# Performance work log

Measured on AMD Instinct MI355X. Metric: run time of the kernel, lower is better.

Reference implementation:

```python
import jax, jax.numpy as jnp
import numpy as np

C_NUM, D_NUM = 64, 128
N_NODES = C_NUM * D_NUM + C_NUM + D_NUM  # 8384
HEADS, OUT = 4, 256


def gat_conv(h, src, dst, W, al, ar, b):
    """DGL-style GATConv (eval mode, attn_drop off). h:[N,F], W:[F,H*O], al/ar:[H,O], b:[H*O]."""
    N = h.shape[0]
    H, O = al.shape
    feat = (h @ W).reshape(N, H, O)
    el = jnp.sum(feat * al, axis=-1)                      # [N,H]
    er = jnp.sum(feat * ar, axis=-1)
    e = jax.nn.leaky_relu(el[src] + er[dst], 0.2)         # [E,H]
    m = jax.ops.segment_max(e, dst, num_segments=N)
    m = jnp.where(jnp.isfinite(m), m, 0.0)
    p = jnp.exp(e - m[dst])
    s = jax.ops.segment_sum(p, dst, num_segments=N)
    a = p / jnp.maximum(s[dst], 1e-9)                     # edge softmax per dst, per head
    out = jax.ops.segment_sum(a[:, :, None] * feat[src], dst, num_segments=N)  # [N,H,O]
    return out + b.reshape(1, H, O)


def cagat_layer(edges, dfeat, cvec, gw, al, ar, gb,
                wq_w, wq_b, wk_w, wk_b, wv_w, wv_b, ip_w, ip_b, op_w, op_b):
    ch = cvec.shape[1]
    pad = jnp.repeat(cvec, D_NUM, axis=0)                       # [c*d, ch]
    pad3 = jnp.broadcast_to(cvec.mean(axis=0), (D_NUM, ch))      # [d, ch]
    cfin = jnp.concatenate([pad, cvec, pad3], axis=0)            # [N, ch]
    inf = jnp.concatenate([dfeat, cfin], axis=1)                 # [N, F+ch]
    # 4 relation-specific GATConvs, stacked (HeteroGraphConv aggregate='stack')
    rst = jnp.stack([gat_conv(inf, edges[t, 0], edges[t, 1], gw[t], al[t], ar[t], gb[t])
                     for t in range(4)], axis=1)                 # [N,4,H,O]
    N = inf.shape[0]
    rst = rst.reshape(N, 4 * HEADS, OUT)
    E = OUT
    Q = (cfin @ wq_w + wq_b)[:, None, :]                         # [N,1,E]
    K = rst @ wk_w + wk_b                                        # [N,16,E]
    V = rst @ wv_w + wv_b
    # nn.MultiheadAttention(E, 1): in-proj then single-head SDPA then out-proj
    q = Q @ ip_w[:E].T + ip_b[:E]
    k = K @ ip_w[E:2 * E].T + ip_b[E:2 * E]
    v = V @ ip_w[2 * E:].T + ip_b[2 * E:]
    att = jax.nn.softmax(jnp.einsum('nqe,nke->nqk', q, k) / jnp.sqrt(jnp.float32(E)), axis=-1)
    o = jnp.einsum('nqk,nke->nqe', att, v) @ op_w.T + op_b
    return o.reshape(N, E)


def setup_inputs() -> dict:
    key = jax.random.key(0)
    ks = iter(jax.random.split(key, 64))
    rn = lambda shape: jax.random.normal(next(ks), shape, jnp.float32) * 0.05
    inp = {}
    inp['x'] = rn((D_NUM, 256))
    inp['cf'] = rn((C_NUM, 512))
    inp['cf_net_w'] = rn((512, 128)); inp['cf_net_b'] = rn((128,))
    inp['ht_w'] = rn((512, 256)); inp['ht_b'] = rn((256,))
    for l in ('1', '2'):
        inp['gw' + l] = rn((4, 384, HEADS * OUT))
        inp['al' + l] = rn((4, HEADS, OUT))
        inp['ar' + l] = rn((4, HEADS, OUT))
        inp['gb' + l] = rn((4, HEADS * OUT))
        inp['wq' + l + '_w'] = rn((128, 256)); inp['wq' + l + '_b'] = rn((256,))
        inp['wk' + l + '_w'] = rn((256, 256)); inp['wk' + l + '_b'] = rn((256,))
        inp['wv' + l + '_w'] = rn((256, 256)); inp['wv' + l + '_b'] = rn((256,))
        inp['ip' + l + '_w'] = rn((768, 256)); inp['ip' + l + '_b'] = rn((768,))
        inp['op' + l + '_w'] = rn((256, 256)); inp['op' + l + '_b'] = rn((256,))
    inp['edges'] = jax.random.randint(next(ks), (4, 2, 50000), 0, N_NODES, dtype=jnp.int32)
    return inp


def reference(x, cf, cf_net_w, cf_net_b, ht_w, ht_b,
              gw1, al1, ar1, gb1, wq1_w, wq1_b, wk1_w, wk1_b, wv1_w, wv1_b, ip1_w, ip1_b, op1_w, op1_b,
              gw2, al2, ar2, gb2, wq2_w, wq2_b, wk2_w, wk2_b, wv2_w, wv2_b, ip2_w, ip2_b, op2_w, op2_b,
              edges):
    cf_vec = cf @ cf_net_w + cf_net_b                           # [c, cell_hidden]
    d_pad = jnp.tile(x, (C_NUM, 1))                             # [c*d, in]
    d_uc = cf @ ht_w + ht_b                                     # [c, in]
    d_feat = jnp.concatenate([d_pad, d_uc, x], axis=0)          # [N, in]
    h = cagat_layer(edges, d_feat, cf_vec, gw1, al1, ar1, gb1,
                    wq1_w, wq1_b, wk1_w, wk1_b, wv1_w, wv1_b, ip1_w, ip1_b, op1_w, op1_b)
    h = cagat_layer(edges, h, cf_vec, gw2, al2, ar2, gb2,
                    wq2_w, wq2_b, wk2_w, wk2_b, wv2_w, wv2_b, ip2_w, ip2_b, op2_w, op2_b)
    return h
```

## Files before the change

### kernel.cpp

```cpp
#include <hip/hip_runtime.h>
#include <hip/hip_bf16.h>

typedef __hip_bfloat16 bf16;
typedef __attribute__((ext_vector_type(8))) short short8;
typedef __attribute__((ext_vector_type(4))) short short4v;
typedef __attribute__((ext_vector_type(4))) float f32x4;

#define KN 8384
#define KNPAD 8448
#define KE 50000
#define NBIG 4480

__device__ __forceinline__ float toF(float v){ return v; }
__device__ __forceinline__ float toF(bf16 v){ return __bfloat162float(v); }
__device__ __forceinline__ float b2f(short u){ return __uint_as_float(((unsigned int)(unsigned short)u) << 16); }
__device__ __forceinline__ void stor(float* p, float v){ *p = v; }
__device__ __forceinline__ void stor(bf16* p, float v){ *p = __float2bfloat16(v); }

__device__ __forceinline__ void glds16(const bf16* g, bf16* l){
  __builtin_amdgcn_global_load_lds(
      (const __attribute__((address_space(1))) unsigned int*)(g),
      (__attribute__((address_space(3))) unsigned int*)(l), 16, 0, 0);
}

template<typename TC>
__global__ __launch_bounds__(256)
void gemm_mfma_bt(const bf16* __restrict__ A, const bf16* __restrict__ BT,
                  const float* __restrict__ bias, TC* __restrict__ C,
                  int M, int N, int K, int ldc, int nbx)
{
  __shared__ bf16 As[3][128 * 32];
  __shared__ bf16 Bs[3][128 * 32];
  const int nwg = gridDim.x;
  const int q = nwg >> 3, r = nwg & 7;
  const int xcd = blockIdx.x & 7, idx = blockIdx.x >> 3;
  const int sw = (xcd < r) ? xcd * (q + 1) + idx : r * (q + 1) + (xcd - r) * q + idx;
  const int bn = (sw % nbx) * 128, bm = (sw / nbx) * 128;
  const int tid = threadIdx.x;
  const int w = tid >> 6, l = tid & 63;
  const int wr = (w >> 1) * 64, wc = (w & 1) * 64;
  const int lr = l & 15;
  int rS[2], lqS[2];
  #pragma unroll
  for (int i = 0; i < 2; i++){
    rS[i] = w * 32 + i * 16 + (l >> 2);
    lqS[i] = (l & 3) ^ ((rS[i] >> 1) & 3);
  }
  const bf16* gA0 = A  + (size_t)(bm + rS[0]) * K + lqS[0] * 8;
  const bf16* gA1 = A  + (size_t)(bm + rS[1]) * K + lqS[1] * 8;
  const bf16* gB0 = BT + (size_t)(bn + rS[0]) * K + lqS[0] * 8;
  const bf16* gB1 = BT + (size_t)(bn + rS[1]) * K + lqS[1] * 8;
  const int nt = K >> 5;
  auto issue = [&](int t){
    int b = t - (t / 3) * 3;
    int k0 = t << 5;
    glds16(gA0 + k0, &As[b][w * 1024]);
    glds16(gA1 + k0, &As[b][w * 1024 + 512]);
    glds16(gB0 + k0, &Bs[b][w * 1024]);
    glds16(gB1 + k0, &Bs[b][w * 1024 + 512]);
  };
  f32x4 acc[4][4] = {};
  issue(0);
  issue(1);
  for (int t = 0; t < nt; t++){
    if (t < nt - 1) asm volatile("s_waitcnt vmcnt(4)\ns_barrier" ::: "memory");
    else            asm volatile("s_waitcnt vmcnt(0)\ns_barrier" ::: "memory");
    int b = t - (t / 3) * 3;
    short8 a[4], bb[4];
    #pragma unroll
    for (int i = 0; i < 4; i++){
      int R = wr + i * 16 + lr;
      int pq = (l >> 4) ^ ((R >> 1) & 3);
      a[i] = *(short8*)&As[b][R * 32 + pq * 8];
    }
    #pragma unroll
    for (int j = 0; j < 4; j++){
      int R = wc + j * 16 + lr;
      int pq = (l >> 4) ^ ((R >> 1) & 3);
      bb[j] = *(short8*)&Bs[b][R * 32 + pq * 8];
    }
    #pragma unroll
    for (int i = 0; i < 4; i++)
      #pragma unroll
      for (int j = 0; j < 4; j++)
        acc[i][j] = __builtin_amdgcn_mfma_f32_16x16x32_bf16(a[i], bb[j], acc[i][j], 0, 0, 0);
    if (t + 2 < nt) issue(t + 2);
  }
  const int orow = (l >> 4) * 4, ocol = l & 15;
  #pragma unroll
  for (int i = 0; i < 4; i++){
    #pragma unroll
    for (int j = 0; j < 4; j++){
      int gcol = bn + wc + j * 16 + ocol;
      float bv = bias ? bias[gcol] : 0.f;
      #pragma unroll
      for (int rg = 0; rg < 4; rg++){
        int grow = bm + wr + i * 16 + orow + rg;
        if (grow < M) stor(&C[(size_t)grow * ldc + gcol], acc[i][j][rg] + bv);
      }
    }
  }
}

__global__ void k_transGW(const float* __restrict__ gw, bf16* __restrict__ bigBT){
  __shared__ float t[32][33];
  int rel = blockIdx.z;
  const float* B = gw + (size_t)rel * 384 * 1024;
  bf16* BT = bigBT + (size_t)rel * 1024 * 384;
  int n0 = blockIdx.x * 32, k0 = blockIdx.y * 32;
  int tx = threadIdx.x, ty = threadIdx.y;
  for (int i = ty; i < 32; i += 8)
    t[i][tx] = B[(size_t)(k0 + i) * 1024 + n0 + tx];
  __syncthreads();
  for (int i = ty; i < 32; i += 8)
    BT[(size_t)(n0 + i) * 384 + k0 + tx] = __float2bfloat16(t[tx][i]);
}

__global__ __launch_bounds__(256)
void k_galr(const float* __restrict__ gw, const float* __restrict__ al,
            const float* __restrict__ ar, bf16* __restrict__ bigBT){
  int r = blockIdx.y;
  int k = blockIdx.x * 4 + (threadIdx.x >> 6);
  int lane = threadIdx.x & 63;
  int rr = r & 15, t = rr >> 2, h = rr & 3;
  const float* wsrc = ((r < 16) ? al : ar) + t * 1024 + h * 256;
  const float* gp = gw + (size_t)t * 384 * 1024 + (size_t)k * 1024 + h * 256;
  float v = 0.f;
  #pragma unroll
  for (int i = 0; i < 4; i++){
    int o = lane + i * 64;
    v += gp[o] * wsrc[o];
  }
  #pragma unroll
  for (int off = 32; off; off >>= 1) v += __shfl_down(v, off);
  if (lane == 0) bigBT[(size_t)(4352 + r) * 384 + k] = __float2bfloat16(v);
}

__global__ void k_zpad(bf16* bigBT){
  int i = blockIdx.x * blockDim.x + threadIdx.x;
  if (i < 96 * 384) bigBT[(size_t)4384 * 384 + i] = __float2bfloat16(0.f);
}

__global__ void k_wprep(const float* __restrict__ ipw, const float* __restrict__ wkw,
                        const float* __restrict__ opw, const float* __restrict__ wvw,
                        float* __restrict__ ipwQT, float* __restrict__ wkwT,
                        float* __restrict__ opwT, float* __restrict__ wvwT){
  __shared__ float t[32][33];
  const float* S; float* D;
  switch (blockIdx.z){
    case 0: S = ipw; D = ipwQT; break;
    case 1: S = wkw; D = wkwT; break;
    case 2: S = opw; D = opwT; break;
    default: S = wvw; D = wvwT; break;
  }
  int c0 = blockIdx.x * 32, r0 = blockIdx.y * 32;
  int tx = threadIdx.x, ty = threadIdx.y;
  for (int i = ty; i < 32; i += 8)
    t[i][tx] = S[(size_t)(r0 + i) * 256 + c0 + tx];
  __syncthreads();
  for (int i = ty; i < 32; i += 8)
    D[(size_t)(c0 + i) * 256 + r0 + tx] = t[tx][i];
}

__global__ __launch_bounds__(256)
void k_fold1(const float* __restrict__ wqw, const float* __restrict__ wqb,
             const float* __restrict__ ipw, const float* __restrict__ ipb,
             const float* __restrict__ ipwQT, const float* __restrict__ wkwT,
             const float* __restrict__ opwT,
             float* __restrict__ Wq, float* __restrict__ B2,
             float* __restrict__ M1, float* __restrict__ bq){
  int b = blockIdx.x, tid = threadIdx.x;
  if (b < 128){
    int c = b; float s = 0.f;
    for (int e = 0; e < 256; e++) s += wqw[c * 256 + e] * ipwQT[e * 256 + tid];
    Wq[c * 256 + tid] = s;
  } else if (b < 384){
    int j = b - 128; float s = 0.f;
    for (int e = 0; e < 256; e++) s += wkwT[e * 256 + tid] * ipw[(256 + j) * 256 + e];
    B2[j * 256 + tid] = s;
  } else if (b < 640){
    int e = b - 384; float s = 0.f;
    for (int f = 0; f < 256; f++) s += ipw[(512 + f) * 256 + e] * opwT[f * 256 + tid];
    M1[e * 256 + tid] = s;
  } else {
    float s = 0.f;
    for (int e = 0; e < 256; e++) s += wqb[e] * ipwQT[e * 256 + tid];
    bq[tid] = s + ipb[tid];
  }
}

__global__ __launch_bounds__(256)
void k_fold2(const float* __restrict__ Wq, const float* __restrict__ B2,
             const float* __restrict__ M1, const float* __restrict__ bq,
             const float* __restrict__ wvb, const float* __restrict__ ipb,
             const float* __restrict__ opb,
             const float* __restrict__ wvwT, const float* __restrict__ opwT,
             bf16* __restrict__ bigBT, bf16* __restrict__ WvT,
             float* __restrict__ bv, float* __restrict__ biasc){
  int b = blockIdx.x, tid = threadIdx.x;
  if (b < 256){
    int d = b; float s = 0.f;
    for (int j = 0; j < 256; j++) s += Wq[d * 256 + j] * B2[j * 256 + tid];
    bigBT[(size_t)(4096 + tid) * 384 + 256 + d] = __float2bfloat16(s);
  } else if (b < 512){
    int j = b - 256; float s = 0.f;
    for (int e = 0; e < 256; e++) s += wvwT[e * 256 + tid] * M1[e * 256 + j];
    WvT[j * 256 + tid] = __float2bfloat16(s);
  } else {
    float b2 = 0.f;
    for (int j = 0; j < 256; j++) b2 += bq[j] * B2[j * 256 + tid];
    float s = 0.f;
    for (int e = 0; e < 256; e++) s += wvb[e] * M1[e * 256 + tid];
    for (int f = 0; f < 256; f++) s += ipb[512 + f] * opwT[f * 256 + tid];
    bv[tid] = s + opb[tid];
    for (int i = tid; i < NBIG; i += 256)
      biasc[i] = (i - 4096 == tid) ? b2 : 0.f;
    for (int k = 0; k < 256; k++)
      bigBT[(size_t)(4096 + tid) * 384 + k] = __float2bfloat16(0.f);
  }
}

__global__ __launch_bounds__(384)
void k_pre(const float* __restrict__ cf, const float* __restrict__ cfw, const float* __restrict__ cfb,
           const float* __restrict__ htw, const float* __restrict__ htb,
           float* __restrict__ cfvec, float* __restrict__ duc)
{
  int c = blockIdx.x;
  int col = threadIdx.x;
  __shared__ float row[512];
  for (int i = col; i < 512; i += 384) row[i] = cf[c * 512 + i];
  __syncthreads();
  if (col < 128){
    float acc = cfb[col];
    for (int k = 0; k < 512; k++) acc += row[k] * cfw[k * 128 + col];
    cfvec[c * 128 + col] = acc;
  } else {
    int j = col - 128;
    float acc = htb[j];
    for (int k = 0; k < 512; k++) acc += row[k] * htw[k * 256 + j];
    duc[c * 256 + j] = acc;
  }
}
__global__ void k_mean(const float* cv, float* m){
  int o = threadIdx.x;
  float s = 0.f;
  for (int c = 0; c < 64; c++) s += cv[c * 128 + o];
  m[o] = s * (1.f / 64.f);
}
__global__ __launch_bounds__(384)
void k_infasm(const float* __restrict__ x, const float* __restrict__ duc,
              const float* __restrict__ cv, const float* __restrict__ cm,
              bf16* __restrict__ inf){
  int n = blockIdx.x, o = threadIdx.x;
  float v;
  if (o < 256){
    if (n < 8192)      v = x[(n & 127) * 256 + o];
    else if (n < 8256) v = duc[(n - 8192) * 256 + o];
    else               v = x[(n - 8256) * 256 + o];
  } else {
    int oo = o - 256;
    if (n < 8192)      v = cv[(n >> 7) * 128 + oo];
    else if (n < 8256) v = cv[(n - 8192) * 128 + oo];
    else               v = cm[oo];
  }
  inf[(size_t)n * 384 + o] = __float2bfloat16(v);
}
__global__ void k_zeroi(int* p, int n){
  int i = blockIdx.x * blockDim.x + threadIdx.x; if (i < n) p[i] = 0;
}
__global__ void k_copyi(const int* a, int* b, int n){
  int i = blockIdx.x * blockDim.x + threadIdx.x; if (i < n) b[i] = a[i];
}
__global__ void k_countB(const int* __restrict__ edges, int* __restrict__ cnt){
  int i = blockIdx.x * blockDim.x + threadIdx.x;
  if (i < 4 * KE){
    int t = i / KE, idx = i - t * KE;
    int d = edges[t * 2 * KE + KE + idx];
    atomicAdd(&cnt[t * KN + d], 1);
  }
}
__global__ void k_fillB(const int* __restrict__ edges, int* __restrict__ cur, int* __restrict__ csrc){
  int i = blockIdx.x * blockDim.x + threadIdx.x;
  if (i < 4 * KE){
    int t = i / KE, idx = i - t * KE;
    int s = edges[t * 2 * KE + idx];
    int d = edges[t * 2 * KE + KE + idx];
    int p = atomicAdd(&cur[t * KN + d], 1);
    csrc[p] = s;
  }
}
__global__ void k_scan(const int* __restrict__ cnt, int* __restrict__ ptr, int n){
  __shared__ int part[1024];
  int tid = threadIdx.x;
  const int CH = (n + 1023) >> 10;
  int base = tid * CH;
  int s = 0;
  for (int i = 0; i < CH; i++){ int idx = base + i; if (idx < n) s += cnt[idx]; }
  part[tid] = s; __syncthreads();
  for (int off = 1; off < 1024; off <<= 1){
    int v = (tid >= off) ? part[tid - off] : 0;
    __syncthreads();
    part[tid] += v;
    __syncthreads();
  }
  int run = part[tid] - s;
  for (int i = 0; i < CH; i++){
    int idx = base + i;
    if (idx < n){ ptr[idx] = run; run += cnt[idx]; }
  }
  if (tid == 1023) ptr[n] = part[1023];
}

__global__ __launch_bounds__(256)
void k_aggattn(const int* __restrict__ ptr, const int* __restrict__ csrc,
               const bf16* __restrict__ big, const float* __restrict__ gb,
               bf16* __restrict__ rbar)
{
  const int n = blockIdx.x, tid = threadIdx.x;
  const int w = tid >> 6, lane = tid & 63;
  const int t = w;
  const int head = lane >> 4;
  __shared__ float s_rst[16][260];
  __shared__ float s_sc[16];
  __shared__ float sa4[4][64][4];
  __shared__ int ssrcW[4][64];
  const int beg = ptr[t * KN + n], deg = ptr[t * KN + n + 1] - beg;
  short4v e4 = *(const short4v*)&big[(size_t)n * NBIG + 4368 + t * 4];
  float ern[4] = {b2f(e4[0]), b2f(e4[1]), b2f(e4[2]), b2f(e4[3])};
  float sums[4] = {0.f, 0.f, 0.f, 0.f};
  for (int j = lane; j < deg; j += 64){
    int s = csrc[beg + j];
    short4v l4 = *(const short4v*)&big[(size_t)s * NBIG + 4352 + t * 4];
    #pragma unroll
    for (int h = 0; h < 4; h++){
      float e = b2f(l4[h]) + ern[h];
      e = e > 0.f ? e : 0.2f * e;
      sums[h] += __expf(e);
    }
  }
  #pragma unroll
  for (int off = 32; off; off >>= 1){
    #pragma unroll
    for (int h = 0; h < 4; h++) sums[h] += __shfl_xor(sums[h], off);
  }
  float sinv[4];
  #pragma unroll
  for (int h = 0; h < 4; h++) sinv[h] = 1.f / fmaxf(sums[h], 1e-9f);
  float acc[16];
  #pragma unroll
  for (int i = 0; i < 16; i++) acc[i] = 0.f;
  const size_t cbase = (size_t)t * 1024 + lane * 16;
  for (int c0 = 0; c0 < deg; c0 += 64){
    int cn = min(64, deg - c0);
    if (lane < cn){
      int s = csrc[beg + c0 + lane];
      ssrcW[t][lane] = s;
      short4v l4 = *(const short4v*)&big[(size_t)s * NBIG + 4352 + t * 4];
      #pragma unroll
      for (int h = 0; h < 4; h++){
        float e = b2f(l4[h]) + ern[h];
        e = e > 0.f ? e : 0.2f * e;
        sa4[t][lane][h] = __expf(e) * sinv[h];
      }
    }
    for (int j = 0; j < cn; j++){
      int s = ssrcW[t][j];
      float wj = sa4[t][j][head];
      const bf16* fp = &big[(size_t)s * NBIG + cbase];
      short8 v0 = *(const short8*)fp;
      short8 v1 = *(const short8*)(fp + 8);
      #pragma unroll
      for (int i = 0; i < 8; i++) acc[i] += wj * b2f(v0[i]);
      #pragma unroll
      for (int i = 0; i < 8; i++) acc[8 + i] += wj * b2f(v1[i]);
    }
  }
  {
    const float* gbp = gb + t * 1024 + lane * 16;
    float* rp = &s_rst[t * 4 + head][(lane & 15) * 16];
    #pragma unroll
    for (int i = 0; i < 16; i++) rp[i] = acc[i] + gbp[i];
  }
  __syncthreads();
  const bf16* q = big + (size_t)n * NBIG + 4096;
  #pragma unroll
  for (int si = 0; si < 4; si++){
    int s = w * 4 + si;
    float v = 0.f;
    #pragma unroll
    for (int i = 0; i < 4; i++){
      int o = lane + i * 64;
      v += s_rst[s][o] * toF(q[o]);
    }
    #pragma unroll
    for (int off = 32; off; off >>= 1) v += __shfl_down(v, off);
    if (lane == 0) s_sc[s] = v * 0.0625f;
  }
  __syncthreads();
  float sc[16]; float m = -1e30f;
  #pragma unroll
  for (int s = 0; s < 16; s++){ sc[s] = s_sc[s]; m = fmaxf(m, sc[s]); }
  float sum = 0.f;
  #pragma unroll
  for (int s = 0; s < 16; s++){ sc[s] = __expf(sc[s] - m); sum += sc[s]; }
  float inv = 1.f / sum;
  float r = 0.f;
  #pragma unroll
  for (int s = 0; s < 16; s++) r += sc[s] * s_rst[s][tid];
  rbar[(size_t)n * 256 + tid] = __float2bfloat16(r * inv);
}

struct LWT {
  const float *gw, *al, *ar, *gb, *wqw, *wqb, *wkw, *wkb, *wvw, *wvb, *ipw, *ipb, *opw, *opb;
};

extern "C" void kernel_launch(void* const* d_in, const int* in_sizes, int n_in,
                              void* d_out, int out_size, void* d_ws, size_t ws_size,
                              hipStream_t stream)
{
  const float* x   = (const float*)d_in[0];
  const float* cf  = (const float*)d_in[1];
  const float* cfw = (const float*)d_in[2];
  const float* cfb = (const float*)d_in[3];
  const float* htw = (const float*)d_in[4];
  const float* htb = (const float*)d_in[5];
  LWT L[2];
  for (int l = 0; l < 2; l++){
    int b = 6 + l * 14;
    L[l].gw  = (const float*)d_in[b + 0];
    L[l].al  = (const float*)d_in[b + 1];
    L[l].ar  = (const float*)d_in[b + 2];
    L[l].gb  = (const float*)d_in[b + 3];
    L[l].wqw = (const float*)d_in[b + 4];
    L[l].wqb = (const float*)d_in[b + 5];
    L[l].wkw = (const float*)d_in[b + 6];
    L[l].wkb = (const float*)d_in[b + 7];
    L[l].wvw = (const float*)d_in[b + 8];
    L[l].wvb = (const float*)d_in[b + 9];
    L[l].ipw = (const float*)d_in[b + 10];
    L[l].ipb = (const float*)d_in[b + 11];
    L[l].opw = (const float*)d_in[b + 12];
    L[l].opb = (const float*)d_in[b + 13];
  }
  const int* edges = (const int*)d_in[34];

  char* w = (char*)d_ws;
  size_t off = 0;
  auto alc = [&](size_t bytes) -> void* {
    off = (off + 255) & ~(size_t)255;
    void* p = w + off; off += bytes; return p;
  };
  float* f_cfvec = (float*)alc(64 * 128 * 4);
  float* f_cfmean= (float*)alc(128 * 4);
  float* f_duc   = (float*)alc(64 * 256 * 4);
  bf16*  b_inf   = (bf16*) alc((size_t)KNPAD * 384 * 2);
  bf16*  b_big   = (bf16*) alc((size_t)KN * NBIG * 2);
  bf16*  b_bigBT = (bf16*) alc((size_t)NBIG * 384 * 2);
  float* f_biasc = (float*)alc((size_t)NBIG * 4);
  bf16*  b_rbar  = (bf16*) alc((size_t)KNPAD * 256 * 2);
  float* f_Wq    = (float*)alc(128 * 256 * 4);
  float* f_B2    = (float*)alc(256 * 256 * 4);
  float* f_M1    = (float*)alc(256 * 256 * 4);
  float* f_bq    = (float*)alc(256 * 4);
  float* f_bv    = (float*)alc(256 * 4);
  bf16*  b_WvT   = (bf16*) alc(256 * 256 * 2);
  float* f_ipwQT = (float*)alc(256 * 256 * 4);
  float* f_wkwT  = (float*)alc(256 * 256 * 4);
  float* f_opwT  = (float*)alc(256 * 256 * 4);
  float* f_wvwT  = (float*)alc(256 * 256 * 4);
  int*   i_ptr   = (int*)  alc((size_t)(4 * KN + 1) * 4);
  int*   i_src   = (int*)  alc((size_t)4 * KE * 4);
  int*   i_cnt   = (int*)  alc((size_t)4 * KN * 4);
  int*   i_cur   = (int*)  alc((size_t)4 * KN * 4);
  if (off > ws_size) return;

  k_pre<<<64, 384, 0, stream>>>(cf, cfw, cfb, htw, htb, f_cfvec, f_duc);
  k_mean<<<1, 128, 0, stream>>>(f_cfvec, f_cfmean);
  k_infasm<<<KN, 384, 0, stream>>>(x, f_duc, f_cfvec, f_cfmean, b_inf);
  k_zpad<<<(96 * 384 + 255) / 256, 256, 0, stream>>>(b_bigBT);

  k_zeroi<<<(4 * KN + 255) / 256, 256, 0, stream>>>(i_cnt, 4 * KN);
  k_countB<<<(4 * KE + 255) / 256, 256, 0, stream>>>(edges, i_cnt);
  k_scan<<<1, 1024, 0, stream>>>(i_cnt, i_ptr, 4 * KN);
  k_copyi<<<(4 * KN + 255) / 256, 256, 0, stream>>>(i_ptr, i_cur, 4 * KN);
  k_fillB<<<(4 * KE + 255) / 256, 256, 0, stream>>>(edges, i_cur, i_src);

  auto run_layer = [&](const LWT& Wt, bool last){
    k_transGW<<<dim3(32, 12, 4), dim3(32, 8), 0, stream>>>(Wt.gw, b_bigBT);
    k_galr<<<dim3(96, 32), 256, 0, stream>>>(Wt.gw, Wt.al, Wt.ar, b_bigBT);
    k_wprep<<<dim3(8, 8, 4), dim3(32, 8), 0, stream>>>(Wt.ipw, Wt.wkw, Wt.opw, Wt.wvw,
                                                       f_ipwQT, f_wkwT, f_opwT, f_wvwT);
    k_fold1<<<641, 256, 0, stream>>>(Wt.wqw, Wt.wqb, Wt.ipw, Wt.ipb,
                                     f_ipwQT, f_wkwT, f_opwT,
                                     f_Wq, f_B2, f_M1, f_bq);
    k_fold2<<<513, 256, 0, stream>>>(f_Wq, f_B2, f_M1, f_bq, Wt.wvb, Wt.ipb, Wt.opb,
                                     f_wvwT, f_opwT,
                                     b_bigBT, b_WvT, f_bv, f_biasc);
    gemm_mfma_bt<bf16><<<(NBIG / 128) * 66, 256, 0, stream>>>(
        b_inf, b_bigBT, f_biasc, b_big, KN, NBIG, 384, NBIG, NBIG / 128);
    k_aggattn<<<KN, 256, 0, stream>>>(i_ptr, i_src, b_big, Wt.gb, b_rbar);
    if (last)
      gemm_mfma_bt<float><<<2 * 66, 256, 0, stream>>>(
          b_rbar, b_WvT, f_bv, (float*)d_out, KN, 256, 256, 256, 2);
    else
      gemm_mfma_bt<bf16><<<2 * 66, 256, 0, stream>>>(
          b_rbar, b_WvT, f_bv, b_inf, KN, 256, 256, 384, 2);
  };

  run_layer(L[0], false);
  run_layer(L[1], true);
}
```

Baseline: 545.4 us.

## Batch both layers' weight prep into merged kernels and unroll edge aggregation

The transpose, al/ar projection, zero-padding and weight-transpose kernels are merged into one `k_prep_all` launch. That launch, plus the fold kernels, now covers both layers at once through a z-dimension over separate per-layer buffers, so all weight preprocessing runs up front with fewer launches. The GEMM K-loop issues the next async LDS load right after the barrier, before the MFMAs, to overlap more. The CSR cursor copy is folded into the scan kernel. The edge gather in aggregation is unrolled by 4 to keep more loads in flight, and `k_fold2` caches a `Wq` row in shared memory. The cost is extra workspace for duplicated per-layer weight buffers.

```diff
diff --git a/kernel.cpp b/kernel.cpp
--- a/kernel.cpp
+++ b/kernel.cpp
@@ -65,6 +65,7 @@
   for (int t = 0; t < nt; t++){
     if (t < nt - 1) asm volatile("s_waitcnt vmcnt(4)\ns_barrier" ::: "memory");
     else            asm volatile("s_waitcnt vmcnt(0)\ns_barrier" ::: "memory");
+    if (t + 2 < nt) issue(t + 2);
     int b = t - (t / 3) * 3;
     short8 a[4], bb[4];
     #pragma unroll
@@ -84,7 +85,6 @@
       #pragma unroll
       for (int j = 0; j < 4; j++)
         acc[i][j] = __builtin_amdgcn_mfma_f32_16x16x32_bf16(a[i], bb[j], acc[i][j], 0, 0, 0);
-    if (t + 2 < nt) issue(t + 2);
   }
   const int orow = (l >> 4) * 4, ocol = l & 15;
   #pragma unroll
@@ -102,121 +102,129 @@
   }
 }
 
-__global__ void k_transGW(const float* __restrict__ gw, bf16* __restrict__ bigBT){
-  __shared__ float t[32][33];
-  int rel = blockIdx.z;
-  const float* B = gw + (size_t)rel * 384 * 1024;
-  bf16* BT = bigBT + (size_t)rel * 1024 * 384;
-  int n0 = blockIdx.x * 32, k0 = blockIdx.y * 32;
-  int tx = threadIdx.x, ty = threadIdx.y;
-  for (int i = ty; i < 32; i += 8)
-    t[i][tx] = B[(size_t)(k0 + i) * 1024 + n0 + tx];
-  __syncthreads();
-  for (int i = ty; i < 32; i += 8)
-    BT[(size_t)(n0 + i) * 384 + k0 + tx] = __float2bfloat16(t[tx][i]);
-}
-
+struct LPtrs {
+  const float *gw[2], *al[2], *ar[2];
+  const float *wqw[2], *wqb[2], *wkw[2], *wvw[2], *wvb[2];
+  const float *ipw[2], *ipb[2], *opw[2], *opb[2];
+  bf16* bigBT[2];
+  float *ipwQT[2], *wkwT[2], *opwT[2], *wvwT[2];
+  float *Wq[2], *B2[2], *M1[2], *bq[2];
+  bf16* WvT[2];
+  float *bv[2], *biasc[2];
+};
+
+#define PT0 1536
+#define PT1 4608
+#define PT2 4864
+#define PT3 5248
+#define PT4 5392
 __global__ __launch_bounds__(256)
-void k_galr(const float* __restrict__ gw, const float* __restrict__ al,
-            const float* __restrict__ ar, bf16* __restrict__ bigBT){
-  int r = blockIdx.y;
-  int k = blockIdx.x * 4 + (threadIdx.x >> 6);
-  int lane = threadIdx.x & 63;
-  int rr = r & 15, t = rr >> 2, h = rr & 3;
-  const float* wsrc = ((r < 16) ? al : ar) + t * 1024 + h * 256;
-  const float* gp = gw + (size_t)t * 384 * 1024 + (size_t)k * 1024 + h * 256;
-  float v = 0.f;
-  #pragma unroll
-  for (int i = 0; i < 4; i++){
-    int o = lane + i * 64;
-    v += gp[o] * wsrc[o];
-  }
-  #pragma unroll
-  for (int off = 32; off; off >>= 1) v += __shfl_down(v, off);
-  if (lane == 0) bigBT[(size_t)(4352 + r) * 384 + k] = __float2bfloat16(v);
-}
-
-__global__ void k_zpad(bf16* bigBT){
-  int i = blockIdx.x * blockDim.x + threadIdx.x;
-  if (i < 96 * 384) bigBT[(size_t)4384 * 384 + i] = __float2bfloat16(0.f);
-}
-
-__global__ void k_wprep(const float* __restrict__ ipw, const float* __restrict__ wkw,
-                        const float* __restrict__ opw, const float* __restrict__ wvw,
-                        float* __restrict__ ipwQT, float* __restrict__ wkwT,
-                        float* __restrict__ opwT, float* __restrict__ wvwT){
-  __shared__ float t[32][33];
-  const float* S; float* D;
-  switch (blockIdx.z){
-    case 0: S = ipw; D = ipwQT; break;
-    case 1: S = wkw; D = wkwT; break;
-    case 2: S = opw; D = opwT; break;
-    default: S = wvw; D = wvwT; break;
-  }
-  int c0 = blockIdx.x * 32, r0 = blockIdx.y * 32;
-  int tx = threadIdx.x, ty = threadIdx.y;
-  for (int i = ty; i < 32; i += 8)
-    t[i][tx] = S[(size_t)(r0 + i) * 256 + c0 + tx];
-  __syncthreads();
-  for (int i = ty; i < 32; i += 8)
-    D[(size_t)(c0 + i) * 256 + r0 + tx] = t[tx][i];
+void k_prep_all(LPtrs P){
+  const int lay = blockIdx.z;
+  const int b = blockIdx.x, tid = threadIdx.x;
+  bf16* bigBT = P.bigBT[lay];
+  if (b < PT0){
+    __shared__ float t[32][33];
+    int rel = b / 384, rem = b % 384;
+    int n0 = (rem % 32) * 32, k0 = (rem / 32) * 32;
+    const float* B = P.gw[lay] + (size_t)rel * 384 * 1024;
+    bf16* BT = bigBT + (size_t)rel * 1024 * 384;
+    int tx = tid & 31, ty = tid >> 5;
+    for (int i = ty; i < 32; i += 8)
+      t[i][tx] = B[(size_t)(k0 + i) * 1024 + n0 + tx];
+    __syncthreads();
+    for (int i = ty; i < 32; i += 8)
+      BT[(size_t)(n0 + i) * 384 + k0 + tx] = __float2bfloat16(t[tx][i]);
+  } else if (b < PT1){
+    int bb = b - PT0;
+    int kblk = bb % 96, r = bb / 96;
+    int k = kblk * 4 + (tid >> 6), lane = tid & 63;
+    int rr = r & 15, t = rr >> 2, h = rr & 3;
+    const float* wsrc = ((r < 16) ? P.al[lay] : P.ar[lay]) + t * 1024 + h * 256;
+    const float* gp = P.gw[lay] + (size_t)t * 384 * 1024 + (size_t)k * 1024 + h * 256;
+    float v = 0.f;
+    #pragma unroll
+    for (int i = 0; i < 4; i++){
+      int o = lane + i * 64;
+      v += gp[o] * wsrc[o];
+    }
+    #pragma unroll
+    for (int off = 32; off; off >>= 1) v += __shfl_down(v, off);
+    if (lane == 0) bigBT[(size_t)(4352 + r) * 384 + k] = __float2bfloat16(v);
+  } else if (b < PT2){
+    __shared__ float t[32][33];
+    int bb = b - PT1;
+    int mat = bb >> 6, rem = bb & 63;
+    int c0 = (rem & 7) * 32, r0 = (rem >> 3) * 32;
+    const float* S; float* D;
+    switch (mat){
+      case 0: S = P.ipw[lay]; D = P.ipwQT[lay]; break;
+      case 1: S = P.wkw[lay]; D = P.wkwT[lay]; break;
+      case 2: S = P.opw[lay]; D = P.opwT[lay]; break;
+      default: S = P.wvw[lay]; D = P.wvwT[lay]; break;
+    }
+    int tx = tid & 31, ty = tid >> 5;
+    for (int i = ty; i < 32; i += 8)
+      t[i][tx] = S[(size_t)(r0 + i) * 256 + c0 + tx];
+    __syncthreads();
+    for (int i = ty; i < 32; i += 8)
+      D[(size_t)(c0 + i) * 256 + r0 + tx] = t[tx][i];
+  } else if (b < PT3){
+    int idx = (b - PT2) * 256 + tid;
+    bigBT[(size_t)(4096 + idx / 384) * 384 + idx % 384] = __float2bfloat16(0.f);
+  } else {
+    int idx = (b - PT3) * 256 + tid;
+    bigBT[(size_t)(4384 + idx / 384) * 384 + idx % 384] = __float2bfloat16(0.f);
+  }
 }
 
 __global__ __launch_bounds__(256)
-void k_fold1(const float* __restrict__ wqw, const float* __restrict__ wqb,
-             const float* __restrict__ ipw, const float* __restrict__ ipb,
-             const float* __restrict__ ipwQT, const float* __restrict__ wkwT,
-             const float* __restrict__ opwT,
-             float* __restrict__ Wq, float* __restrict__ B2,
-             float* __restrict__ M1, float* __restrict__ bq){
+void k_fold1(LPtrs P){
+  const int lay = blockIdx.z;
   int b = blockIdx.x, tid = threadIdx.x;
   if (b < 128){
     int c = b; float s = 0.f;
-    for (int e = 0; e < 256; e++) s += wqw[c * 256 + e] * ipwQT[e * 256 + tid];
-    Wq[c * 256 + tid] = s;
+    for (int e = 0; e < 256; e++) s += P.wqw[lay][c * 256 + e] * P.ipwQT[lay][e * 256 + tid];
+    P.Wq[lay][c * 256 + tid] = s;
   } else if (b < 384){
     int j = b - 128; float s = 0.f;
-    for (int e = 0; e < 256; e++) s += wkwT[e * 256 + tid] * ipw[(256 + j) * 256 + e];
-    B2[j * 256 + tid] = s;
+    for (int e = 0; e < 256; e++) s += P.wkwT[lay][e * 256 + tid] * P.ipw[lay][(256 + j) * 256 + e];
+    P.B2[lay][j * 256 + tid] = s;
   } else if (b < 640){
     int e = b - 384; float s = 0.f;
-    for (int f = 0; f < 256; f++) s += ipw[(512 + f) * 256 + e] * opwT[f * 256 + tid];
-    M1[e * 256 + tid] = s;
+    for (int f = 0; f < 256; f++) s += P.ipw[lay][(512 + f) * 256 + e] * P.opwT[lay][f * 256 + tid];
+    P.M1[lay][e * 256 + tid] = s;
   } else {
     float s = 0.f;
-    for (int e = 0; e < 256; e++) s += wqb[e] * ipwQT[e * 256 + tid];
-    bq[tid] = s + ipb[tid];
+    for (int e = 0; e < 256; e++) s += P.wqb[lay][e] * P.ipwQT[lay][e * 256 + tid];
+    P.bq[lay][tid] = s + P.ipb[lay][tid];
   }
 }
 
 __global__ __launch_bounds__(256)
-void k_fold2(const float* __restrict__ Wq, const float* __restrict__ B2,
-             const float* __restrict__ M1, const float* __restrict__ bq,
-             const float* __restrict__ wvb, const float* __restrict__ ipb,
-             const float* __restrict__ opb,
-             const float* __restrict__ wvwT, const float* __restrict__ opwT,
-             bf16* __restrict__ bigBT, bf16* __restrict__ WvT,
-             float* __restrict__ bv, float* __restrict__ biasc){
+void k_fold2(LPtrs P){
+  const int lay = blockIdx.z;
   int b = blockIdx.x, tid = threadIdx.x;
   if (b < 256){
-    int d = b; float s = 0.f;
-    for (int j = 0; j < 256; j++) s += Wq[d * 256 + j] * B2[j * 256 + tid];
-    bigBT[(size_t)(4096 + tid) * 384 + 256 + d] = __float2bfloat16(s);
+    __shared__ float wqr[256];
+    wqr[tid] = P.Wq[lay][b * 256 + tid];
+    __syncthreads();
+    float s = 0.f;
+    for (int j = 0; j < 256; j++) s += wqr[j] * P.B2[lay][j * 256 + tid];
+    P.bigBT[lay][(size_t)(4096 + tid) * 384 + 256 + b] = __float2bfloat16(s);
   } else if (b < 512){
     int j = b - 256; float s = 0.f;
-    for (int e = 0; e < 256; e++) s += wvwT[e * 256 + tid] * M1[e * 256 + j];
-    WvT[j * 256 + tid] = __float2bfloat16(s);
+    for (int e = 0; e < 256; e++) s += P.wvwT[lay][e * 256 + tid] * P.M1[lay][e * 256 + j];
+    P.WvT[lay][j * 256 + tid] = __float2bfloat16(s);
   } else {
     float b2 = 0.f;
-    for (int j = 0; j < 256; j++) b2 += bq[j] * B2[j * 256 + tid];
+    for (int j = 0; j < 256; j++) b2 += P.bq[lay][j] * P.B2[lay][j * 256 + tid];
     float s = 0.f;
-    for (int e = 0; e < 256; e++) s += wvb[e] * M1[e * 256 + tid];
-    for (int f = 0; f < 256; f++) s += ipb[512 + f] * opwT[f * 256 + tid];
-    bv[tid] = s + opb[tid];
+    for (int e = 0; e < 256; e++) s += P.wvb[lay][e] * P.M1[lay][e * 256 + tid];
+    for (int f = 0; f < 256; f++) s += P.ipb[lay][512 + f] * P.opwT[lay][f * 256 + tid];
+    P.bv[lay][tid] = s + P.opb[lay][tid];
     for (int i = tid; i < NBIG; i += 256)
-      biasc[i] = (i - 4096 == tid) ? b2 : 0.f;
-    for (int k = 0; k < 256; k++)
-      bigBT[(size_t)(4096 + tid) * 384 + k] = __float2bfloat16(0.f);
+      P.biasc[lay][i] = (i - 4096 == tid) ? b2 : 0.f;
   }
 }
 
@@ -268,9 +276,6 @@
 __global__ void k_zeroi(int* p, int n){
   int i = blockIdx.x * blockDim.x + threadIdx.x; if (i < n) p[i] = 0;
 }
-__global__ void k_copyi(const int* a, int* b, int n){
-  int i = blockIdx.x * blockDim.x + threadIdx.x; if (i < n) b[i] = a[i];
-}
 __global__ void k_countB(const int* __restrict__ edges, int* __restrict__ cnt){
   int i = blockIdx.x * blockDim.x + threadIdx.x;
   if (i < 4 * KE){
@@ -289,7 +294,8 @@
     csrc[p] = s;
   }
 }
-__global__ void k_scan(const int* __restrict__ cnt, int* __restrict__ ptr, int n){
+__global__ void k_scan(const int* __restrict__ cnt, int* __restrict__ ptr,
+                       int* __restrict__ cur, int n){
   __shared__ int part[1024];
   int tid = threadIdx.x;
   const int CH = (n + 1023) >> 10;
@@ -306,7 +312,7 @@
   int run = part[tid] - s;
   for (int i = 0; i < CH; i++){
     int idx = base + i;
-    if (idx < n){ ptr[idx] = run; run += cnt[idx]; }
+    if (idx < n){ ptr[idx] = run; cur[idx] = run; run += cnt[idx]; }
   }
   if (tid == 1023) ptr[n] = part[1023];
 }
@@ -363,7 +369,28 @@
         sa4[t][lane][h] = __expf(e) * sinv[h];
       }
     }
-    for (int j = 0; j < cn; j++){
+    int j = 0;
+    for (; j + 3 < cn; j += 4){
+      int s0 = ssrcW[t][j],     s1 = ssrcW[t][j + 1];
+      int s2 = ssrcW[t][j + 2], s3 = ssrcW[t][j + 3];
+      float w0 = sa4[t][j][head],     w1 = sa4[t][j + 1][head];
+      float w2 = sa4[t][j + 2][head], w3 = sa4[t][j + 3][head];
+      const bf16* f0 = &big[(size_t)s0 * NBIG + cbase];
+      const bf16* f1 = &big[(size_t)s1 * NBIG + cbase];
+      const bf16* f2 = &big[(size_t)s2 * NBIG + cbase];
+      const bf16* f3 = &big[(size_t)s3 * NBIG + cbase];
+      short8 a0 = *(const short8*)f0, b0 = *(const short8*)(f0 + 8);
+      short8 a1 = *(const short8*)f1, b1 = *(const short8*)(f1 + 8);
+      short8 a2 = *(const short8*)f2, b2 = *(const short8*)(f2 + 8);
+      short8 a3 = *(const short8*)f3, b3 = *(const short8*)(f3 + 8);
+      #pragma unroll
+      for (int i = 0; i < 8; i++)
+        acc[i] += w0 * b2f(a0[i]) + w1 * b2f(a1[i]) + w2 * b2f(a2[i]) + w3 * b2f(a3[i]);
+      #pragma unroll
+      for (int i = 0; i < 8; i++)
+        acc[8 + i] += w0 * b2f(b0[i]) + w1 * b2f(b1[i]) + w2 * b2f(b2[i]) + w3 * b2f(b3[i]);
+    }
+    for (; j < cn; j++){
       int s = ssrcW[t][j];
       float wj = sa4[t][j][head];
       const bf16* fp = &big[(size_t)s * NBIG + cbase];
@@ -409,10 +436,6 @@
   for (int s = 0; s < 16; s++) r += sc[s] * s_rst[s][tid];
   rbar[(size_t)n * 256 + tid] = __float2bfloat16(r * inv);
 }
-
-struct LWT {
-  const float *gw, *al, *ar, *gb, *wqw, *wqb, *wkw, *wkb, *wvw, *wvb, *ipw, *ipb, *opw, *opb;
-};
 
 extern "C" void kernel_launch(void* const* d_in, const int* in_sizes, int n_in,
                               void* d_out, int out_size, void* d_ws, size_t ws_size,
@@ -424,23 +447,23 @@
   const float* cfb = (const float*)d_in[3];
   const float* htw = (const float*)d_in[4];
   const float* htb = (const float*)d_in[5];
-  LWT L[2];
+  LPtrs P;
+  const float* gbp[2];
   for (int l = 0; l < 2; l++){
     int b = 6 + l * 14;
-    L[l].gw  = (const float*)d_in[b + 0];
-    L[l].al  = (const float*)d_in[b + 1];
-    L[l].ar  = (const float*)d_in[b + 2];
-    L[l].gb  = (const float*)d_in[b + 3];
-    L[l].wqw = (const float*)d_in[b + 4];
-    L[l].wqb = (const float*)d_in[b + 5];
-    L[l].wkw = (const float*)d_in[b + 6];
-    L[l].wkb = (const float*)d_in[b + 7];
-    L[l].wvw = (const float*)d_in[b + 8];
-    L[l].wvb = (const float*)d_in[b + 9];
-    L[l].ipw = (const float*)d_in[b + 10];
-    L[l].ipb = (const float*)d_in[b + 11];
-    L[l].opw = (const float*)d_in[b + 12];
-    L[l].opb = (const float*)d_in[b + 13];
+    P.gw[l]  = (const float*)d_in[b + 0];
+    P.al[l]  = (const float*)d_in[b + 1];
+    P.ar[l]  = (const float*)d_in[b + 2];
+    gbp[l]   = (const float*)d_in[b + 3];
+    P.wqw[l] = (const float*)d_in[b + 4];
+    P.wqb[l] = (const float*)d_in[b + 5];
+    P.wkw[l] = (const float*)d_in[b + 6];
+    P.wvw[l] = (const float*)d_in[b + 8];
+    P.wvb[l] = (const float*)d_in[b + 9];
+    P.ipw[l] = (const float*)d_in[b + 10];
+    P.ipb[l] = (const float*)d_in[b + 11];
+    P.opw[l] = (const float*)d_in[b + 12];
+    P.opb[l] = (const float*)d_in[b + 13];
   }
   const int* edges = (const int*)d_in[34];
 
@@ -455,58 +478,48 @@
   float* f_duc   = (float*)alc(64 * 256 * 4);
   bf16*  b_inf   = (bf16*) alc((size_t)KNPAD * 384 * 2);
   bf16*  b_big   = (bf16*) alc((size_t)KN * NBIG * 2);
-  bf16*  b_bigBT = (bf16*) alc((size_t)NBIG * 384 * 2);
-  float* f_biasc = (float*)alc((size_t)NBIG * 4);
   bf16*  b_rbar  = (bf16*) alc((size_t)KNPAD * 256 * 2);
-  float* f_Wq    = (float*)alc(128 * 256 * 4);
-  float* f_B2    = (float*)alc(256 * 256 * 4);
-  float* f_M1    = (float*)alc(256 * 256 * 4);
-  float* f_bq    = (float*)alc(256 * 4);
-  float* f_bv    = (float*)alc(256 * 4);
-  bf16*  b_WvT   = (bf16*) alc(256 * 256 * 2);
-  float* f_ipwQT = (float*)alc(256 * 256 * 4);
-  float* f_wkwT  = (float*)alc(256 * 256 * 4);
-  float* f_opwT  = (float*)alc(256 * 256 * 4);
-  float* f_wvwT  = (float*)alc(256 * 256 * 4);
-  int*   i_ptr   = (int*)  alc((size_t)(4 * KN + 1) * 4);
-  int*   i_src   = (int*)  alc((size_t)4 * KE * 4);
-  int*   i_cnt   = (int*)  alc((size_t)4 * KN * 4);
-  int*   i_cur   = (int*)  alc((size_t)4 * KN * 4);
+  for (int l = 0; l < 2; l++){
+    P.bigBT[l] = (bf16*) alc((size_t)NBIG * 384 * 2);
+    P.biasc[l] = (float*)alc((size_t)NBIG * 4);
+    P.ipwQT[l] = (float*)alc(256 * 256 * 4);
+    P.wkwT[l]  = (float*)alc(256 * 256 * 4);
+    P.opwT[l]  = (float*)alc(256 * 256 * 4);
+    P.wvwT[l]  = (float*)alc(256 * 256 * 4);
+    P.Wq[l]    = (float*)alc(128 * 256 * 4);
+    P.B2[l]    = (float*)alc(256 * 256 * 4);
+    P.M1[l]    = (float*)alc(256 * 256 * 4);
+    P.bq[l]    = (float*)alc(256 * 4);
+    P.bv[l]    = (float*)alc(256 * 4);
+    P.WvT[l]   = (bf16*) alc(256 * 256 * 2);
+  }
+  int* i_ptr = (int*)alc((size_t)(4 * KN + 1) * 4);
+  int* i_src = (int*)alc((size_t)4 * KE * 4);
+  int* i_cnt = (int*)alc((size_t)4 * KN * 4);
+  int* i_cur = (int*)alc((size_t)4 * KN * 4);
   if (off > ws_size) return;
 
   k_pre<<<64, 384, 0, stream>>>(cf, cfw, cfb, htw, htb, f_cfvec, f_duc);
   k_mean<<<1, 128, 0, stream>>>(f_cfvec, f_cfmean);
   k_infasm<<<KN, 384, 0, stream>>>(x, f_duc, f_cfvec, f_cfmean, b_inf);
-  k_zpad<<<(96 * 384 + 255) / 256, 256, 0, stream>>>(b_bigBT);
+  k_prep_all<<<dim3(PT4, 1, 2), 256, 0, stream>>>(P);
+  k_fold1<<<dim3(641, 1, 2), 256, 0, stream>>>(P);
+  k_fold2<<<dim3(513, 1, 2), 256, 0, stream>>>(P);
 
   k_zeroi<<<(4 * KN + 255) / 256, 256, 0, stream>>>(i_cnt, 4 * KN);
   k_countB<<<(4 * KE + 255) / 256, 256, 0, stream>>>(edges, i_cnt);
-  k_scan<<<1, 1024, 0, stream>>>(i_cnt, i_ptr, 4 * KN);
-  k_copyi<<<(4 * KN + 255) / 256, 256, 0, stream>>>(i_ptr, i_cur, 4 * KN);
+  k_scan<<<1, 1024, 0, stream>>>(i_cnt, i_ptr, i_cur, 4 * KN);
   k_fillB<<<(4 * KE + 255) / 256, 256, 0, stream>>>(edges, i_cur, i_src);
 
-  auto run_layer = [&](const LWT& Wt, bool last){
-    k_transGW<<<dim3(32, 12, 4), dim3(32, 8), 0, stream>>>(Wt.gw, b_bigBT);
-    k_galr<<<dim3(96, 32), 256, 0, stream>>>(Wt.gw, Wt.al, Wt.ar, b_bigBT);
-    k_wprep<<<dim3(8, 8, 4), dim3(32, 8), 0, stream>>>(Wt.ipw, Wt.wkw, Wt.opw, Wt.wvw,
-                                                       f_ipwQT, f_wkwT, f_opwT, f_wvwT);
-    k_fold1<<<641, 256, 0, stream>>>(Wt.wqw, Wt.wqb, Wt.ipw, Wt.ipb,
-                                     f_ipwQT, f_wkwT, f_opwT,
-                                     f_Wq, f_B2, f_M1, f_bq);
-    k_fold2<<<513, 256, 0, stream>>>(f_Wq, f_B2, f_M1, f_bq, Wt.wvb, Wt.ipb, Wt.opb,
-                                     f_wvwT, f_opwT,
-                                     b_bigBT, b_WvT, f_bv, f_biasc);
+  for (int l = 0; l < 2; l++){
     gemm_mfma_bt<bf16><<<(NBIG / 128) * 66, 256, 0, stream>>>(
-        b_inf, b_bigBT, f_biasc, b_big, KN, NBIG, 384, NBIG, NBIG / 128);
-    k_aggattn<<<KN, 256, 0, stream>>>(i_ptr, i_src, b_big, Wt.gb, b_rbar);
-    if (last)
+        b_inf, P.bigBT[l], P.biasc[l], b_big, KN, NBIG, 384, NBIG, NBIG / 128);
+    k_aggattn<<<KN, 256, 0, stream>>>(i_ptr, i_src, b_big, gbp[l], b_rbar);
+    if (l == 1)
       gemm_mfma_bt<float><<<2 * 66, 256, 0, stream>>>(
-          b_rbar, b_WvT, f_bv, (float*)d_out, KN, 256, 256, 256, 2);
+          b_rbar, P.WvT[l], P.bv[l], (float*)d_out, KN, 256, 256, 256, 2);
     else
       gemm_mfma_bt<bf16><<<2 * 66, 256, 0, stream>>>(
-          b_rbar, b_WvT, f_bv, b_inf, KN, 256, 256, 384, 2);
-  };
-
-  run_layer(L[0], false);
-  run_layer(L[1], true);
-}
+          b_rbar, P.WvT[l], P.bv[l], b_inf, KN, 256, 256, 384, 2);
+  }
+}
```

Measured after the change: 521.0 us. 1.05x faster.
